# Optimization experiments

Hardware: AMD Instinct MI355X
Metric: run time of the kernel (lower is better)

## Reference

```python
import jax, jax.numpy as jnp
import numpy as np

N_NODES = 100000
N_EDGES = 1600000
DIM = 64
N_LAYERS = 6


def setup_inputs() -> dict:
    key = jax.random.key(0)
    ks = jax.random.split(key, 4)
    x = jax.random.normal(ks[0], (N_NODES, DIM), dtype=jnp.float32)
    edge_index = jax.random.randint(ks[1], (2, N_EDGES), 0, N_NODES, dtype=jnp.int64)
    # SAGEConv params per layer: lin_l (neighbor, with bias), lin_r (root, no bias)
    Wl = jax.random.normal(ks[2], (N_LAYERS, DIM, DIM), dtype=jnp.float32) * 0.05
    bl = jnp.zeros((N_LAYERS, DIM), dtype=jnp.float32)
    Wr = jax.random.normal(ks[3], (N_LAYERS, DIM, DIM), dtype=jnp.float32) * 0.05
    return {"x": x, "edge_index": edge_index, "Wl": Wl, "bl": bl, "Wr": Wr}


def reference(x, edge_index, Wl, bl, Wr):
    src, dst = edge_index[0], edge_index[1]
    n = x.shape[0]

    def sage(h, W_l, b_l, W_r):
        # gather neighbor features [E, D], scatter-max into dst nodes [N, D]
        agg = jax.ops.segment_max(h[src], dst, num_segments=n)
        # nodes with no in-edges get -inf from segment_max -> 0 (PyG convention)
        agg = jnp.where(jnp.isneginf(agg), jnp.zeros((), h.dtype), agg)
        return agg @ W_l.T + b_l + h @ W_r.T

    h = x
    for i in range(N_LAYERS):
        h = sage(h, Wl[i], bl[i], Wr[i])
        if i < N_LAYERS - 1:
            h = jax.nn.relu(h)
        # dropout (p=0.1) is identity in eval mode
    return h
```

## Files before the change

kernel.cpp:

```cpp
#include <hip/hip_runtime.h>
#include <hip/hip_bf16.h>
#include <math.h>

#define DIM 64

typedef _Float16 half_t;
typedef __attribute__((ext_vector_type(8))) _Float16 half8;
typedef __attribute__((ext_vector_type(4))) _Float16 h16x4;
typedef __attribute__((ext_vector_type(4))) float f32x4;

__device__ __forceinline__ half8 hmax8(half8 a, half8 b) {
    return __builtin_elementwise_max(a, b);
}


__global__ void kbcnt(const int* __restrict__ ei, int E, int* __restrict__ gcnt) {
    __shared__ int h[256];
    int t = threadIdx.x;
    h[t] = 0;
    __syncthreads();
    for (int e = blockIdx.x * 256 + t; e < E; e += gridDim.x * 256)
        atomicAdd(&h[ei[E + e] >> 9], 1);
    __syncthreads();
    if (h[t]) atomicAdd(&gcnt[t], h[t]);
}

__global__ void kbscan(const int* __restrict__ gcnt, int* __restrict__ gbs,
                       int* __restrict__ gbc, int NB, int E,
                       int* __restrict__ rs, int N) {
    __shared__ int sm[256];
    int t = threadIdx.x;
    int v = (t < NB) ? gcnt[t] : 0;
    sm[t] = v;
    __syncthreads();
    for (int off = 1; off < 256; off <<= 1) {
        int add = (t >= off) ? sm[t - off] : 0;
        __syncthreads();
        sm[t] += add;
        __syncthreads();
    }
    int excl = sm[t] - v;
    if (t < NB) { gbs[t] = excl; gbc[t] = excl; }
    if (t == NB - 1) gbs[NB] = excl + v;
    if (t == 0) rs[N] = E;
}

__global__ void kbin(const int* __restrict__ ei, int E,
                     int* __restrict__ gbc, int* __restrict__ pairs, int NB) {
    __shared__ int hist[256];
    __shared__ int basep[256];
    const int t = threadIdx.x;
    const int c0 = blockIdx.x * 4096;
    hist[t] = 0;
    __syncthreads();
    int s[16], d[16];
#pragma unroll
    for (int i = 0; i < 16; ++i) {
        int e = c0 + i * 256 + t;
        if (e < E) {
            s[i] = ei[e];
            d[i] = ei[E + e];
            atomicAdd(&hist[d[i] >> 9], 1);
        } else d[i] = -1;
    }
    __syncthreads();
    if (t < NB) {
        basep[t] = atomicAdd(&gbc[t], hist[t]);
        hist[t] = 0;
    }
    __syncthreads();
#pragma unroll
    for (int i = 0; i < 16; ++i) {
        if (d[i] >= 0) {
            int b = d[i] >> 9;
            int off = atomicAdd(&hist[b], 1);
            pairs[basep[b] + off] = (s[i] << 9) | (d[i] & 511);
        }
    }
}

__global__ void __launch_bounds__(256) kfinal(
        const int* __restrict__ pairs, const int* __restrict__ gbs,
        int* __restrict__ rs, int* __restrict__ ssrc, int N) {
    __shared__ int lcnt[512];
    __shared__ int lcur[512];
    __shared__ int ps[256];
    const int b = blockIdx.x;
    const int t = threadIdx.x;
    const int n0 = b << 9;
    const int e0 = gbs[b], e1 = gbs[b + 1];
    lcnt[t] = 0;
    lcnt[t + 256] = 0;
    __syncthreads();
    for (int e = e0 + t; e < e1; e += 256)
        atomicAdd(&lcnt[pairs[e] & 511], 1);
    __syncthreads();
    int c0 = lcnt[2 * t], c1 = lcnt[2 * t + 1];
    int sum = c0 + c1;
    ps[t] = sum;
    __syncthreads();
    for (int off = 1; off < 256; off <<= 1) {
        int add = (t >= off) ? ps[t - off] : 0;
        __syncthreads();
        ps[t] += add;
        __syncthreads();
    }
    int excl = ps[t] - sum;
    lcur[2 * t] = excl;
    lcur[2 * t + 1] = excl + c0;
    int n = n0 + 2 * t;
    if (n < N) rs[n] = e0 + excl;
    if (n + 1 < N) rs[n + 1] = e0 + excl + c0;
    __syncthreads();
    for (int e = e0 + t; e < e1; e += 256) {
        int p = pairs[e];
        int pos = atomicAdd(&lcur[p & 511], 1);
        ssrc[e0 + pos] = (int)((unsigned)p >> 9) << 7;
    }
}


__global__ void kcvt(const float* __restrict__ x, half_t* __restrict__ phi, int n4) {
    int i = blockIdx.x * blockDim.x + threadIdx.x;
    if (i < n4) {
        f32x4 v = ((const f32x4*)x)[i];
        h16x4 hi;
#pragma unroll
        for (int c = 0; c < 4; ++c) hi[c] = (half_t)v[c];
        ((h16x4*)phi)[i] = hi;
    }
}


__global__ void kprepw(const float* __restrict__ Wl, const float* __restrict__ Wr,
                       half_t* __restrict__ Bf) {
    int id = blockIdx.x * blockDim.x + threadIdx.x;
    if (id >= 6 * 4 * 4 * 64 * 8) return;
    int i = id & 7;
    int lane = (id >> 3) & 63;
    int t = (id >> 9) & 3;
    int s = (id >> 11) & 3;
    int layer = id >> 13;
    int k = s * 32 + (lane >> 4) * 8 + i;
    int j = t * 16 + (lane & 15);
    float v = (k < 64) ? Wl[(layer * 64 + j) * 64 + k]
                       : Wr[(layer * 64 + j) * 64 + (k - 64)];
    half_t hi = (half_t)v;
    half_t lo = (half_t)(v - (float)hi);
    int f = (s * 4 + t) * 2;
    int base = layer * 16384 + f * 512 + lane * 8 + i;
    Bf[base] = hi;
    Bf[base + 512] = lo;
}


__global__ void __launch_bounds__(256) kagg(
        const half_t* __restrict__ h16, const int* __restrict__ rs,
        const int* __restrict__ soff, half_t* __restrict__ agg16, int N) {
    int lane = threadIdx.x & 63;
    int wv = (blockIdx.x * blockDim.x + threadIdx.x) >> 6;
    int row = wv * 8 + (lane >> 3);
    int sub = lane & 7;
    if (row >= N) return;
    const char* hb = (const char*)h16 + sub * 16;
    int beg = rs[row], end = rs[row + 1];
    int lastE = end - 1;
    const half_t NEG = (half_t)(-65504.0f);
    half8 m0 = {NEG, NEG, NEG, NEG, NEG, NEG, NEG, NEG};
    half8 m1 = m0, m2 = m0, m3 = m0;
    for (int e = beg; e < end; e += 4) {
        int e1 = (e + 1 <= lastE) ? e + 1 : lastE;
        int e2 = (e + 2 <= lastE) ? e + 2 : lastE;
        int e3 = (e + 3 <= lastE) ? e + 3 : lastE;
        int o0 = soff[e], o1 = soff[e1], o2 = soff[e2], o3 = soff[e3];
        m0 = hmax8(m0, *(const half8*)(hb + o0));
        m1 = hmax8(m1, *(const half8*)(hb + o1));
        m2 = hmax8(m2, *(const half8*)(hb + o2));
        m3 = hmax8(m3, *(const half8*)(hb + o3));
    }
    half8 m = hmax8(hmax8(m0, m1), hmax8(m2, m3));
    if (end <= beg) {
        half8 z = {(half_t)0.f, (half_t)0.f, (half_t)0.f, (half_t)0.f,
                   (half_t)0.f, (half_t)0.f, (half_t)0.f, (half_t)0.f};
        m = z;
    }
    *(half8*)((char*)agg16 + (size_t)row * 128 + sub * 16) = m;
}


__global__ void __launch_bounds__(256, 2) kgemm(
        const half_t* __restrict__ agg16, const half_t* __restrict__ hin,
        const half_t* __restrict__ Bf, const float* __restrict__ bias,
        float* __restrict__ out32, half_t* __restrict__ hout, int N, int last) {
    const int lane = threadIdx.x & 63;
    const int quad = lane >> 4;
    const int lrow = lane & 15;
    const int wv = (blockIdx.x * blockDim.x + threadIdx.x) >> 6;
    const int nwv = (gridDim.x * blockDim.x) >> 6;
    const int ntiles = (N + 15) >> 4;

    const half8* __restrict__ Bp = (const half8*)Bf;
    half8 bh[4][4], bl[4][4];
#pragma unroll
    for (int s = 0; s < 4; ++s)
#pragma unroll
        for (int t = 0; t < 4; ++t) {
            int f = (s * 4 + t) * 2;
            bh[s][t] = Bp[f * 64 + lane];
            bl[s][t] = Bp[f * 64 + 64 + lane];
        }

    float bs[4];
#pragma unroll
    for (int t = 0; t < 4; ++t) bs[t] = bias[t * 16 + lrow];

    for (int tile = wv; tile < ntiles; tile += nwv) {
        const int m0 = tile << 4;
        int row = m0 + lrow;
        if (row >= N) row = N - 1;
        const char* pa = (const char*)agg16 + (size_t)row * 128 + quad * 16;
        const char* ph = (const char*)hin   + (size_t)row * 128 + quad * 16;
        half8 Aa0 = *(const half8*)(pa);
        half8 Aa1 = *(const half8*)(pa + 64);
        half8 Hh0 = *(const half8*)(ph);
        half8 Hh1 = *(const half8*)(ph + 64);

        f32x4 acc[4] = {{0.f, 0.f, 0.f, 0.f}, {0.f, 0.f, 0.f, 0.f},
                        {0.f, 0.f, 0.f, 0.f}, {0.f, 0.f, 0.f, 0.f}};
#pragma unroll
        for (int t = 0; t < 4; ++t) {
            acc[t] = __builtin_amdgcn_mfma_f32_16x16x32_f16(Aa0, bh[0][t], acc[t], 0, 0, 0);
            acc[t] = __builtin_amdgcn_mfma_f32_16x16x32_f16(Aa0, bl[0][t], acc[t], 0, 0, 0);
            acc[t] = __builtin_amdgcn_mfma_f32_16x16x32_f16(Aa1, bh[1][t], acc[t], 0, 0, 0);
            acc[t] = __builtin_amdgcn_mfma_f32_16x16x32_f16(Aa1, bl[1][t], acc[t], 0, 0, 0);
            acc[t] = __builtin_amdgcn_mfma_f32_16x16x32_f16(Hh0, bh[2][t], acc[t], 0, 0, 0);
            acc[t] = __builtin_amdgcn_mfma_f32_16x16x32_f16(Hh0, bl[2][t], acc[t], 0, 0, 0);
            acc[t] = __builtin_amdgcn_mfma_f32_16x16x32_f16(Hh1, bh[3][t], acc[t], 0, 0, 0);
            acc[t] = __builtin_amdgcn_mfma_f32_16x16x32_f16(Hh1, bl[3][t], acc[t], 0, 0, 0);
        }

#pragma unroll
        for (int t = 0; t < 4; ++t) {
            int col = t * 16 + lrow;
#pragma unroll
            for (int r = 0; r < 4; ++r) {
                int orow = m0 + quad * 4 + r;
                if (orow < N) {
                    float v = acc[t][r] + bs[t];
                    if (!last) {
                        v = fmaxf(v, 0.0f);
                        hout[(size_t)orow * DIM + col] = (half_t)v;
                    } else {
                        out32[(size_t)orow * DIM + col] = v;
                    }
                }
            }
        }
    }
}


extern "C" void kernel_launch(void* const* d_in, const int* in_sizes, int n_in,
                              void* d_out, int out_size, void* d_ws, size_t ws_size,
                              hipStream_t stream) {
    const float* x  = (const float*)d_in[0];
    const int*   ei = (const int*)d_in[1];
    const float* Wl = (const float*)d_in[2];
    const float* bl = (const float*)d_in[3];
    const float* Wr = (const float*)d_in[4];
    int N = in_sizes[0] / DIM;
    int E = in_sizes[1] / 2;

    size_t nd = (size_t)N * DIM;
    half_t* p0    = (half_t*)d_ws;
    half_t* p1    = p0 + nd;
    half_t* agg16 = p1 + nd;
    int*    rs    = (int*)(agg16 + nd);
    int*    ssrc  = rs + (N + 4);
    int*    gcnt  = ssrc + E;
    int*    gbs   = gcnt + 256;
    int*    gbc   = gbs + 260;
    half_t* Bf    = (half_t*)(gbc + 256);

    int NB = (N + 511) >> 9;
    int* pairs = (int*)agg16;

    hipMemsetAsync(gcnt, 0, 256 * sizeof(int), stream);
    kbcnt<<<640, 256, 0, stream>>>(ei, E, gcnt);
    kbscan<<<1, 256, 0, stream>>>(gcnt, gbs, gbc, NB, E, rs, N);
    kbin<<<(E + 4095) / 4096, 256, 0, stream>>>(ei, E, gbc, pairs, NB);
    kfinal<<<NB, 256, 0, stream>>>(pairs, gbs, rs, ssrc, N);
    kprepw<<<(6 * 4 * 4 * 64 * 8 + 255) / 256, 256, 0, stream>>>(Wl, Wr, Bf);
    kcvt<<<((int)(nd / 4) + 255) / 256, 256, 0, stream>>>(x, p0, (int)(nd / 4));

    for (int l = 0; l < 6; ++l) {
        half_t* ih = (l & 1) ? p1 : p0;
        half_t* oh = (l & 1) ? p0 : p1;
        int last = (l == 5);
        kagg<<<(N + 31) / 32, 256, 0, stream>>>(ih, rs, ssrc, agg16, N);
        kgemm<<<512, 256, 0, stream>>>(agg16, ih, Bf + l * 16384, bl + l * 64,
                                       (float*)d_out, oh, N, last);
    }
}
```

Baseline: 393.0 us.

## Fuse neighbor max-aggregation into the MFMA GEMM kernel

The separate gather/scatter-max kernel is removed and the per-row neighbor max is now computed inside the GEMM kernel's tile loop. Each quad of lanes gathers two 16-byte chunks per edge, and the result feeds the MFMA A operand directly from registers. This drops the fp16 aggregation buffer write and read and one launch per layer. In exchange, the latency-bound gather now runs in a persistent grid of 512 blocks capped at two blocks per CU. A wave also covers 16 rows instead of 8, so degree imbalance causes more divergence and less latency hiding.

```diff
diff --git a/kernel.cpp b/kernel.cpp
--- a/kernel.cpp
+++ b/kernel.cpp
@@ -154,44 +154,11 @@
 }
 
 
-__global__ void __launch_bounds__(256) kagg(
-        const half_t* __restrict__ h16, const int* __restrict__ rs,
-        const int* __restrict__ soff, half_t* __restrict__ agg16, int N) {
-    int lane = threadIdx.x & 63;
-    int wv = (blockIdx.x * blockDim.x + threadIdx.x) >> 6;
-    int row = wv * 8 + (lane >> 3);
-    int sub = lane & 7;
-    if (row >= N) return;
-    const char* hb = (const char*)h16 + sub * 16;
-    int beg = rs[row], end = rs[row + 1];
-    int lastE = end - 1;
-    const half_t NEG = (half_t)(-65504.0f);
-    half8 m0 = {NEG, NEG, NEG, NEG, NEG, NEG, NEG, NEG};
-    half8 m1 = m0, m2 = m0, m3 = m0;
-    for (int e = beg; e < end; e += 4) {
-        int e1 = (e + 1 <= lastE) ? e + 1 : lastE;
-        int e2 = (e + 2 <= lastE) ? e + 2 : lastE;
-        int e3 = (e + 3 <= lastE) ? e + 3 : lastE;
-        int o0 = soff[e], o1 = soff[e1], o2 = soff[e2], o3 = soff[e3];
-        m0 = hmax8(m0, *(const half8*)(hb + o0));
-        m1 = hmax8(m1, *(const half8*)(hb + o1));
-        m2 = hmax8(m2, *(const half8*)(hb + o2));
-        m3 = hmax8(m3, *(const half8*)(hb + o3));
-    }
-    half8 m = hmax8(hmax8(m0, m1), hmax8(m2, m3));
-    if (end <= beg) {
-        half8 z = {(half_t)0.f, (half_t)0.f, (half_t)0.f, (half_t)0.f,
-                   (half_t)0.f, (half_t)0.f, (half_t)0.f, (half_t)0.f};
-        m = z;
-    }
-    *(half8*)((char*)agg16 + (size_t)row * 128 + sub * 16) = m;
-}
-
-
-__global__ void __launch_bounds__(256, 2) kgemm(
-        const half_t* __restrict__ agg16, const half_t* __restrict__ hin,
-        const half_t* __restrict__ Bf, const float* __restrict__ bias,
-        float* __restrict__ out32, half_t* __restrict__ hout, int N, int last) {
+__global__ void __launch_bounds__(256, 2) kfused(
+        const half_t* __restrict__ hin, const int* __restrict__ rs,
+        const int* __restrict__ soff, const half_t* __restrict__ Bf,
+        const float* __restrict__ bias, float* __restrict__ out32,
+        half_t* __restrict__ hout, int N, int last) {
     const int lane = threadIdx.x & 63;
     const int quad = lane >> 4;
     const int lrow = lane & 15;
@@ -214,16 +181,44 @@
 #pragma unroll
     for (int t = 0; t < 4; ++t) bs[t] = bias[t * 16 + lrow];
 
+    const char* hq = (const char*)hin + quad * 16;
+    const half_t NEG = (half_t)(-65504.0f);
+
     for (int tile = wv; tile < ntiles; tile += nwv) {
         const int m0 = tile << 4;
         int row = m0 + lrow;
         if (row >= N) row = N - 1;
-        const char* pa = (const char*)agg16 + (size_t)row * 128 + quad * 16;
-        const char* ph = (const char*)hin   + (size_t)row * 128 + quad * 16;
-        half8 Aa0 = *(const half8*)(pa);
-        half8 Aa1 = *(const half8*)(pa + 64);
+
+        const char* ph = (const char*)hin + (size_t)row * 128 + quad * 16;
         half8 Hh0 = *(const half8*)(ph);
         half8 Hh1 = *(const half8*)(ph + 64);
+
+        int beg = rs[row], end = rs[row + 1];
+        int lastE = end - 1;
+        half8 m0a = {NEG, NEG, NEG, NEG, NEG, NEG, NEG, NEG};
+        half8 m1a = m0a, m2a = m0a, m3a = m0a;
+        half8 m0b = m0a, m1b = m0a, m2b = m0a, m3b = m0a;
+        for (int e = beg; e < end; e += 4) {
+            int e1 = (e + 1 <= lastE) ? e + 1 : lastE;
+            int e2 = (e + 2 <= lastE) ? e + 2 : lastE;
+            int e3 = (e + 3 <= lastE) ? e + 3 : lastE;
+            int o0 = soff[e], o1 = soff[e1], o2 = soff[e2], o3 = soff[e3];
+            m0a = hmax8(m0a, *(const half8*)(hq + o0));
+            m0b = hmax8(m0b, *(const half8*)(hq + o0 + 64));
+            m1a = hmax8(m1a, *(const half8*)(hq + o1));
+            m1b = hmax8(m1b, *(const half8*)(hq + o1 + 64));
+            m2a = hmax8(m2a, *(const half8*)(hq + o2));
+            m2b = hmax8(m2b, *(const half8*)(hq + o2 + 64));
+            m3a = hmax8(m3a, *(const half8*)(hq + o3));
+            m3b = hmax8(m3b, *(const half8*)(hq + o3 + 64));
+        }
+        half8 Aa0 = hmax8(hmax8(m0a, m1a), hmax8(m2a, m3a));
+        half8 Aa1 = hmax8(hmax8(m0b, m1b), hmax8(m2b, m3b));
+        if (end <= beg) {
+            half8 z = {(half_t)0.f, (half_t)0.f, (half_t)0.f, (half_t)0.f,
+                       (half_t)0.f, (half_t)0.f, (half_t)0.f, (half_t)0.f};
+            Aa0 = z; Aa1 = z;
+        }
 
         f32x4 acc[4] = {{0.f, 0.f, 0.f, 0.f}, {0.f, 0.f, 0.f, 0.f},
                         {0.f, 0.f, 0.f, 0.f}, {0.f, 0.f, 0.f, 0.f}};
@@ -274,8 +269,8 @@
     size_t nd = (size_t)N * DIM;
     half_t* p0    = (half_t*)d_ws;
     half_t* p1    = p0 + nd;
-    half_t* agg16 = p1 + nd;
-    int*    rs    = (int*)(agg16 + nd);
+    half_t* scratch = p1 + nd;
+    int*    rs    = (int*)(scratch + nd);
     int*    ssrc  = rs + (N + 4);
     int*    gcnt  = ssrc + E;
     int*    gbs   = gcnt + 256;
@@ -283,7 +278,7 @@
     half_t* Bf    = (half_t*)(gbc + 256);
 
     int NB = (N + 511) >> 9;
-    int* pairs = (int*)agg16;
+    int* pairs = (int*)scratch;
 
     hipMemsetAsync(gcnt, 0, 256 * sizeof(int), stream);
     kbcnt<<<640, 256, 0, stream>>>(ei, E, gcnt);
@@ -297,8 +292,7 @@
         half_t* ih = (l & 1) ? p1 : p0;
         half_t* oh = (l & 1) ? p0 : p1;
         int last = (l == 5);
-        kagg<<<(N + 31) / 32, 256, 0, stream>>>(ih, rs, ssrc, agg16, N);
-        kgemm<<<512, 256, 0, stream>>>(agg16, ih, Bf + l * 16384, bl + l * 64,
-                                       (float*)d_out, oh, N, last);
-    }
-}
+        kfused<<<512, 256, 0, stream>>>(ih, rs, ssrc, Bf + l * 16384, bl + l * 64,
+                                        (float*)d_out, oh, N, last);
+    }
+}
```

Result: slower. 442.1 us (+12.5%).
